# Kernel optimization log

Measured on AMD Instinct MI355X. Metric: run time of the kernel, lower is better.

Reference implementation:

```python
import jax, jax.numpy as jnp
import numpy as np
from functools import partial

NUM_CLASSES = 80
NUM_GRID = 32
NUM_BBOX = 2
IMG_H, IMG_W = 448.0, 448.0
IOU_THRESH = 0.5
SCORE_THRESH = 0.1
N_BATCH = 128


def setup_inputs() -> dict:
    key = jax.random.key(0)
    G2 = NUM_GRID * NUM_GRID
    feat = G2 * (NUM_CLASSES + 5 * NUM_BBOX)
    x = jax.random.uniform(key, (N_BATCH, feat), dtype=jnp.float32)
    return {"x": x}


def _decode(bb):
    # bb: [G2, 5] -> [G2, 5] as (x0, y0, x1, y1, conf) in image pixels
    G = NUM_GRID
    idx = jnp.arange(G * G)
    xg = (idx % G).astype(bb.dtype)   # x varies fastest (repeat(G,1).flatten())
    yg = (idx // G).astype(bb.dtype)  # y repeated per row (repeat(1,G).flatten())
    cx = (bb[:, 0] + xg) / G
    cy = (bb[:, 1] + yg) / G
    x0 = (cx - bb[:, 2] / 2) * IMG_W
    y0 = (cy - bb[:, 3] / 2) * IMG_H
    x1 = (cx + bb[:, 2] / 2) * IMG_W
    y1 = (cy + bb[:, 3] / 2) * IMG_H
    return jnp.stack([x0, y0, x1, y1, bb[:, 4]], axis=1)


def _pairwise_iou(boxes):
    # boxes: [M, 4] -> iou [M, M]
    area = jnp.maximum(boxes[:, 2] - boxes[:, 0], 0.0) * jnp.maximum(boxes[:, 3] - boxes[:, 1], 0.0)
    lt = jnp.maximum(boxes[:, None, :2], boxes[None, :, :2])
    rb = jnp.minimum(boxes[:, None, 2:], boxes[None, :, 2:])
    wh = jnp.maximum(rb - lt, 0.0)
    inter = wh[..., 0] * wh[..., 1]
    union = area[:, None] + area[None, :] - inter
    return inter / jnp.maximum(union, 1e-9)


def _nms_keep(iou, valid_sorted, thresh):
    # greedy NMS over score-sorted boxes; suppress j>i when iou[i,j] > thresh
    M = iou.shape[0]
    j = jnp.arange(M)

    def body(i, keep):
        sup = keep[i] & (iou[i] > thresh) & (j > i)
        return keep & ~sup

    return jax.lax.fori_loop(0, M, body, valid_sorted)


def _per_image(logits, bb):
    # logits: [G2, C], bb: [G2, 5]
    probs = jax.nn.softmax(logits, axis=-1)
    dec = _decode(bb)                      # [G2, 5]
    scores = dec[:, 4]
    reserve = scores > SCORE_THRESH        # bool mask (torch filters; we mask)
    # clip boxes to image
    boxes = jnp.stack([
        jnp.clip(dec[:, 0], 0.0, IMG_W),
        jnp.clip(dec[:, 1], 0.0, IMG_H),
        jnp.clip(dec[:, 2], 0.0, IMG_W),
        jnp.clip(dec[:, 3], 0.0, IMG_H),
    ], axis=1)
    labels = jnp.argmax(probs, axis=-1)
    # batched NMS via per-class coordinate offsets (torchvision trick)
    max_coord = jnp.max(jnp.where(reserve[:, None], boxes, 0.0))
    obox = boxes + (labels.astype(boxes.dtype) * (max_coord + 1.0))[:, None]
    eff = jnp.where(reserve, scores, -1.0)
    order = jnp.argsort(-eff)
    iou = _pairwise_iou(obox[order])       # [G2, G2]
    keep_sorted = _nms_keep(iou, reserve[order], IOU_THRESH)
    keep = jnp.zeros_like(reserve).at[order].set(keep_sorted)
    return boxes, scores, reserve, keep


def reference(x):
    N = x.shape[0]
    G2 = NUM_GRID * NUM_GRID
    x = x.reshape(N, G2, NUM_CLASSES + 5 * NUM_BBOX)
    class_logits = x[..., :NUM_CLASSES]                       # [N, G2, C]
    yb = x[..., NUM_CLASSES:].reshape(N, G2, NUM_BBOX, 5)
    best = jnp.argmax(yb[..., 4], axis=-1)                    # [N, G2]
    yolo_bboxes = jnp.take_along_axis(yb, best[..., None, None], axis=2)[:, :, 0, :]  # [N, G2, 5]
    boxes, scores, reserve_mask, keep_mask = jax.vmap(_per_image)(class_logits, yolo_bboxes)
    return class_logits, yolo_bboxes, boxes, scores, reserve_mask, keep_mask
```

## Files before the change

kernel.cpp:

```cpp
#include <hip/hip_runtime.h>
#include <stdint.h>

#define NB 128
#define G 32
#define G2 1024
#define NC 80
#define IMGW 448.0f
#define NCELL (NB * G2)

#define WS_LABEL_OFF 0u
#define WS_SEG_OFF   0x80000u
#define WS_BSEG_OFF  0x180000u
#define WS_CNT_OFF   0x380000u
#define WS_START_OFF 0x38A000u

__global__ __launch_bounds__(256) void percell_kernel(
    const float* __restrict__ x,
    float* __restrict__ out0, float* __restrict__ out1,
    float* __restrict__ out2, float* __restrict__ out3,
    float* __restrict__ out4, float* __restrict__ out5,
    int* __restrict__ ws_label)
{
#pragma clang fp contract(off)
    __shared__ float s_out1[16 * 5];
    __shared__ float4 s_out2[16];
    __shared__ float s_out3[16];
    __shared__ float s_out4[16];
    __shared__ int   s_lab[16];

    const int t = threadIdx.x;
    const int lane = t & 15;
    const int grp  = t >> 4;
    const int l64  = t & 63;
    const int base = l64 & 48;
    const int cell = blockIdx.x * 16 + grp;

    const float2* p2 = (const float2*)x + (size_t)cell * 45;
    float2* o0 = (float2*)out0 + (size_t)cell * 40;

    float bv = -INFINITY;
    int bi = 0;

    float2 a = p2[lane];
    o0[lane] = a;
    if (a.x > bv) { bv = a.x; bi = 2 * lane; }
    if (a.y > bv) { bv = a.y; bi = 2 * lane + 1; }
    float2 bq = p2[lane + 16];
    o0[lane + 16] = bq;
    if (bq.x > bv) { bv = bq.x; bi = 32 + 2 * lane; }
    if (bq.y > bv) { bv = bq.y; bi = 32 + 2 * lane + 1; }
    float2 cq = make_float2(0.0f, 0.0f);
    if (lane < 13) cq = p2[lane + 32];
    if (lane < 8) {
        o0[lane + 32] = cq;
        if (cq.x > bv) { bv = cq.x; bi = 64 + 2 * lane; }
        if (cq.y > bv) { bv = cq.y; bi = 64 + 2 * lane + 1; }
    }

#pragma unroll
    for (int o = 1; o < 16; o <<= 1) {
        float ov = __shfl_xor(bv, o, 64);
        int   oi = __shfl_xor(bi, o, 64);
        if (ov > bv || (ov == bv && oi < bi)) { bv = ov; bi = oi; }
    }

    float f40x = __shfl(cq.x, base + 8, 64),  f40y = __shfl(cq.y, base + 8, 64);
    float f41x = __shfl(cq.x, base + 9, 64),  f41y = __shfl(cq.y, base + 9, 64);
    float f42x = __shfl(cq.x, base + 10, 64), f42y = __shfl(cq.y, base + 10, 64);
    float f43x = __shfl(cq.x, base + 11, 64), f43y = __shfl(cq.y, base + 11, 64);
    float f44x = __shfl(cq.x, base + 12, 64), f44y = __shfl(cq.y, base + 12, 64);

    if (lane == 0) {
        float b0, b1, b2, b3, b4;
        if (f44y > f42x) { b0 = f42y; b1 = f43x; b2 = f43y; b3 = f44x; b4 = f44y; }
        else             { b0 = f40x; b1 = f40y; b2 = f41x; b3 = f41y; b4 = f42x; }

        s_out1[grp * 5 + 0] = b0; s_out1[grp * 5 + 1] = b1;
        s_out1[grp * 5 + 2] = b2; s_out1[grp * 5 + 3] = b3;
        s_out1[grp * 5 + 4] = b4;

        int g = cell & (G2 - 1);
        float xg = (float)(g & (G - 1));
        float yg = (float)(g >> 5);
        float cx = (b0 + xg) / 32.0f;
        float cy = (b1 + yg) / 32.0f;
        float hw = b2 / 2.0f, hh = b3 / 2.0f;
        float x0 = fminf(fmaxf((cx - hw) * IMGW, 0.0f), IMGW);
        float y0 = fminf(fmaxf((cy - hh) * IMGW, 0.0f), IMGW);
        float x1 = fminf(fmaxf((cx + hw) * IMGW, 0.0f), IMGW);
        float y1 = fminf(fmaxf((cy + hh) * IMGW, 0.0f), IMGW);

        s_out2[grp] = make_float4(x0, y0, x1, y1);
        s_out3[grp] = b4;
        s_out4[grp] = (b4 > 0.1f) ? 1.0f : 0.0f;
        s_lab[grp] = bi;
    }
    __syncthreads();

    if (t < 80)                 out1[(size_t)blockIdx.x * 80 + t] = s_out1[t];
    else if (t >= 80 && t < 96) out3[(size_t)blockIdx.x * 16 + (t - 80)] = s_out3[t - 80];
    else if (t < 112)           out4[(size_t)blockIdx.x * 16 + (t - 96)] = s_out4[t - 96];
    else if (t < 128)           ws_label[(size_t)blockIdx.x * 16 + (t - 112)] = s_lab[t - 112];
    else if (t < 144)           ((float4*)out2)[(size_t)blockIdx.x * 16 + (t - 128)] = s_out2[t - 128];
    else if (t < 160)           out5[(size_t)blockIdx.x * 16 + (t - 144)] = 0.0f;
}

__global__ __launch_bounds__(1024) void build_kernel(
    const float4* __restrict__ boxes,
    const float* __restrict__ scores,
    const int* __restrict__ labels,
    unsigned long long* __restrict__ ws_seg,
    float4* __restrict__ ws_bseg,
    int* __restrict__ ws_cnt, int* __restrict__ ws_start)
{
#pragma clang fp contract(off)
    __shared__ unsigned long long seg_s[G2];
    __shared__ float4 bseg_s[G2];
    __shared__ int cnt_s[NC];
    __shared__ int start_s[NC];
    __shared__ int cur_s[NC];
    __shared__ float red_s[16];

    const int n = blockIdx.x;
    const int t = threadIdx.x;

    if (t < NC) { cnt_s[t] = 0; cur_s[t] = 0; }

    float4 b = boxes[n * G2 + t];
    float sc = scores[n * G2 + t];
    int lab = labels[n * G2 + t];
    bool res = sc > 0.1f;

    float m = res ? fmaxf(fmaxf(b.x, b.y), fmaxf(b.z, b.w)) : 0.0f;
#pragma unroll
    for (int o = 32; o > 0; o >>= 1) m = fmaxf(m, __shfl_xor(m, o, 64));
    if ((t & 63) == 0) red_s[t >> 6] = m;
    __syncthreads();
    if (t == 0) {
        float mm = red_s[0];
#pragma unroll
        for (int i = 1; i < 16; ++i) mm = fmaxf(mm, red_s[i]);
        red_s[0] = mm;
    }
    if (res) atomicAdd(&cnt_s[lab], 1);
    __syncthreads();
    const float mult = red_s[0] + 1.0f;

    if (t < NC) {
        int s = 0;
        for (int c = 0; c < t; ++c) s += cnt_s[c];
        start_s[t] = s;
    }
    __syncthreads();

    if (res) {
        int slot = atomicAdd(&cur_s[lab], 1);
        int pos = start_s[lab] + slot;
        seg_s[pos] = ((unsigned long long)__float_as_uint(sc) << 10) |
                     (unsigned)(1023 - t);
        float off = (float)lab * mult;
        bseg_s[pos] = make_float4(b.x + off, b.y + off, b.z + off, b.w + off);
    }
    __syncthreads();

    ws_seg[n * G2 + t]  = seg_s[t];
    ws_bseg[n * G2 + t] = bseg_s[t];
    if (t < NC) {
        ws_cnt[n * NC + t]   = cnt_s[t];
        ws_start[n * NC + t] = start_s[t];
    }
}

__global__ __launch_bounds__(256) void nms_kernel(
    const unsigned long long* __restrict__ ws_seg,
    const float4* __restrict__ ws_bseg,
    const int* __restrict__ ws_cnt, const int* __restrict__ ws_start,
    float* __restrict__ out5)
{
#pragma clang fp contract(off)
    __shared__ unsigned long long k_s[4][64];
    __shared__ float4 ob_s[4][64];
    __shared__ float  ar_s[4][64];

    const int wv = threadIdx.x >> 6;
    const int l  = threadIdx.x & 63;
    const int w  = blockIdx.x * 4 + wv;
    const int n  = w / NC;
    const int c  = w - n * NC;

    const int cnt = ws_cnt[n * NC + c];
    if (cnt == 0) return;
    const int s = ws_start[n * NC + c];

    const bool valid = l < cnt;
    unsigned long long key = 0;
    int idx = 0;
    float4 mob = make_float4(0.f, 0.f, 0.f, 0.f);
    float marea = 0.f;
    if (valid) {
        key = ws_seg[n * G2 + s + l];
        mob = ws_bseg[n * G2 + s + l];
        idx = 1023 - (int)(key & 1023u);
        marea = fmaxf(mob.z - mob.x, 0.0f) * fmaxf(mob.w - mob.y, 0.0f);
        k_s[wv][l] = key;
    }
    asm volatile("s_waitcnt lgkmcnt(0)" ::: "memory");

    int r = 0;
    for (int i = 0; i < cnt; ++i) r += (k_s[wv][i] > key);

    if (valid) { ob_s[wv][r] = mob; ar_s[wv][r] = marea; }
    asm volatile("s_waitcnt lgkmcnt(0)" ::: "memory");

    unsigned long long sup = 0;
    for (int i = 0; i < cnt; ++i) {
        float4 A = ob_s[wv][i];
        float aA = ar_s[wv][i];
        float ltx = fmaxf(A.x, mob.x);
        float lty = fmaxf(A.y, mob.y);
        float rbx = fminf(A.z, mob.z);
        float rby = fminf(A.w, mob.w);
        float ww = fmaxf(rbx - ltx, 0.0f);
        float hh = fmaxf(rby - lty, 0.0f);
        float inter = ww * hh;
        float uni = (aA + marea) - inter;
        float iou = inter / fmaxf(uni, 1e-9f);
        if (i < r && iou > 0.5f) sup |= 1ull << i;
    }

    unsigned long long kept = 0;
    for (int i = 0; i < cnt; ++i) {
        bool ki = (r == i) && ((sup & kept) == 0ull);
        kept |= __ballot(ki) ? (1ull << i) : 0ull;
    }
    if (valid) out5[n * G2 + idx] = ((kept >> r) & 1ull) ? 1.0f : 0.0f;
}

extern "C" void kernel_launch(void* const* d_in, const int* in_sizes, int n_in,
                              void* d_out, int out_size, void* d_ws, size_t ws_size,
                              hipStream_t stream) {
    const float* x = (const float*)d_in[0];
    float* out = (float*)d_out;
    float* out0 = out;
    float* out1 = out0 + (size_t)NCELL * NC;
    float* out2 = out1 + (size_t)NCELL * 5;
    float* out3 = out2 + (size_t)NCELL * 4;
    float* out4 = out3 + (size_t)NCELL;
    float* out5 = out4 + (size_t)NCELL;

    int* ws_label = (int*)((char*)d_ws + WS_LABEL_OFF);
    unsigned long long* ws_seg = (unsigned long long*)((char*)d_ws + WS_SEG_OFF);
    float4* ws_bseg = (float4*)((char*)d_ws + WS_BSEG_OFF);
    int* ws_cnt   = (int*)((char*)d_ws + WS_CNT_OFF);
    int* ws_start = (int*)((char*)d_ws + WS_START_OFF);

    percell_kernel<<<NCELL / 16, 256, 0, stream>>>(
        x, out0, out1, out2, out3, out4, out5, ws_label);
    build_kernel<<<NB, 1024, 0, stream>>>(
        (const float4*)out2, out3, ws_label, ws_seg, ws_bseg, ws_cnt, ws_start);
    nms_kernel<<<(NB * NC) / 4, 256, 0, stream>>>(
        ws_seg, ws_bseg, ws_cnt, ws_start, out5);
}
```

Before: 41.95 us.

## Eliminate build kernel by per-class key scan with ballot compaction in NMS

Percell kernel now emits packed keys (label, score, cell index) and per-block coordinate maxima. The NMS kernel reduces the maxima and has each wavefront scan all keys of its image, compacting its class's entries via ballot/popcount, then gathers boxes and applies the class offset. This removes the separate per-image build kernel and its launch and serialization, at the cost of every class wavefront reading the whole image's key array.

After: 45.64 us. 1.09x slower.

```diff
diff --git a/kernel.cpp b/kernel.cpp
--- a/kernel.cpp
+++ b/kernel.cpp
@@ -8,25 +8,23 @@
 #define IMGW 448.0f
 #define NCELL (NB * G2)
 
-#define WS_LABEL_OFF 0u
-#define WS_SEG_OFF   0x80000u
-#define WS_BSEG_OFF  0x180000u
-#define WS_CNT_OFF   0x380000u
-#define WS_START_OFF 0x38A000u
+#define WS_KEY_OFF  0u
+#define WS_BMAX_OFF 0x100000u
 
 __global__ __launch_bounds__(256) void percell_kernel(
     const float* __restrict__ x,
     float* __restrict__ out0, float* __restrict__ out1,
     float* __restrict__ out2, float* __restrict__ out3,
     float* __restrict__ out4, float* __restrict__ out5,
-    int* __restrict__ ws_label)
+    unsigned long long* __restrict__ ws_key, float* __restrict__ ws_bmax)
 {
 #pragma clang fp contract(off)
     __shared__ float s_out1[16 * 5];
     __shared__ float4 s_out2[16];
     __shared__ float s_out3[16];
     __shared__ float s_out4[16];
-    __shared__ int   s_lab[16];
+    __shared__ unsigned long long s_key[16];
+    __shared__ float s_mx[16];
 
     const int t = threadIdx.x;
     const int lane = t & 15;
@@ -92,89 +90,36 @@
 
         s_out2[grp] = make_float4(x0, y0, x1, y1);
         s_out3[grp] = b4;
-        s_out4[grp] = (b4 > 0.1f) ? 1.0f : 0.0f;
-        s_lab[grp] = bi;
+        bool res = b4 > 0.1f;
+        s_out4[grp] = res ? 1.0f : 0.0f;
+
+        s_key[grp] = res
+            ? (((unsigned long long)bi << 41) |
+               ((unsigned long long)__float_as_uint(b4) << 10) |
+               (unsigned)(1023 - g))
+            : (127ull << 41);
+        s_mx[grp] = res ? fmaxf(fmaxf(x0, y0), fmaxf(x1, y1)) : 0.0f;
     }
     __syncthreads();
 
     if (t < 80)                 out1[(size_t)blockIdx.x * 80 + t] = s_out1[t];
     else if (t >= 80 && t < 96) out3[(size_t)blockIdx.x * 16 + (t - 80)] = s_out3[t - 80];
     else if (t < 112)           out4[(size_t)blockIdx.x * 16 + (t - 96)] = s_out4[t - 96];
-    else if (t < 128)           ws_label[(size_t)blockIdx.x * 16 + (t - 112)] = s_lab[t - 112];
+    else if (t < 128)           ws_key[(size_t)blockIdx.x * 16 + (t - 112)] = s_key[t - 112];
     else if (t < 144)           ((float4*)out2)[(size_t)blockIdx.x * 16 + (t - 128)] = s_out2[t - 128];
     else if (t < 160)           out5[(size_t)blockIdx.x * 16 + (t - 144)] = 0.0f;
+    else if (t == 160) {
+        float mm = s_mx[0];
+#pragma unroll
+        for (int i = 1; i < 16; ++i) mm = fmaxf(mm, s_mx[i]);
+        ws_bmax[blockIdx.x] = mm;
+    }
 }
 
-__global__ __launch_bounds__(1024) void build_kernel(
+__global__ __launch_bounds__(256) void nms_kernel(
+    const unsigned long long* __restrict__ ws_key,
+    const float* __restrict__ ws_bmax,
     const float4* __restrict__ boxes,
-    const float* __restrict__ scores,
-    const int* __restrict__ labels,
-    unsigned long long* __restrict__ ws_seg,
-    float4* __restrict__ ws_bseg,
-    int* __restrict__ ws_cnt, int* __restrict__ ws_start)
-{
-#pragma clang fp contract(off)
-    __shared__ unsigned long long seg_s[G2];
-    __shared__ float4 bseg_s[G2];
-    __shared__ int cnt_s[NC];
-    __shared__ int start_s[NC];
-    __shared__ int cur_s[NC];
-    __shared__ float red_s[16];
-
-    const int n = blockIdx.x;
-    const int t = threadIdx.x;
-
-    if (t < NC) { cnt_s[t] = 0; cur_s[t] = 0; }
-
-    float4 b = boxes[n * G2 + t];
-    float sc = scores[n * G2 + t];
-    int lab = labels[n * G2 + t];
-    bool res = sc > 0.1f;
-
-    float m = res ? fmaxf(fmaxf(b.x, b.y), fmaxf(b.z, b.w)) : 0.0f;
-#pragma unroll
-    for (int o = 32; o > 0; o >>= 1) m = fmaxf(m, __shfl_xor(m, o, 64));
-    if ((t & 63) == 0) red_s[t >> 6] = m;
-    __syncthreads();
-    if (t == 0) {
-        float mm = red_s[0];
-#pragma unroll
-        for (int i = 1; i < 16; ++i) mm = fmaxf(mm, red_s[i]);
-        red_s[0] = mm;
-    }
-    if (res) atomicAdd(&cnt_s[lab], 1);
-    __syncthreads();
-    const float mult = red_s[0] + 1.0f;
-
-    if (t < NC) {
-        int s = 0;
-        for (int c = 0; c < t; ++c) s += cnt_s[c];
-        start_s[t] = s;
-    }
-    __syncthreads();
-
-    if (res) {
-        int slot = atomicAdd(&cur_s[lab], 1);
-        int pos = start_s[lab] + slot;
-        seg_s[pos] = ((unsigned long long)__float_as_uint(sc) << 10) |
-                     (unsigned)(1023 - t);
-        float off = (float)lab * mult;
-        bseg_s[pos] = make_float4(b.x + off, b.y + off, b.z + off, b.w + off);
-    }
-    __syncthreads();
-
-    ws_seg[n * G2 + t]  = seg_s[t];
-    ws_bseg[n * G2 + t] = bseg_s[t];
-    if (t < NC) {
-        ws_cnt[n * NC + t]   = cnt_s[t];
-        ws_start[n * NC + t] = start_s[t];
-    }
-}
-
-__global__ __launch_bounds__(256) void nms_kernel(
-    const unsigned long long* __restrict__ ws_seg,
-    const float4* __restrict__ ws_bseg,
-    const int* __restrict__ ws_cnt, const int* __restrict__ ws_start,
     float* __restrict__ out5)
 {
 #pragma clang fp contract(off)
@@ -188,23 +133,40 @@
     const int n  = w / NC;
     const int c  = w - n * NC;
 
-    const int cnt = ws_cnt[n * NC + c];
+    float m = ws_bmax[n * 64 + l];
+#pragma unroll
+    for (int o = 32; o > 0; o >>= 1) m = fmaxf(m, __shfl_xor(m, o, 64));
+    const float mult = m + 1.0f;
+    const float off = (float)c * mult;
+
+    const unsigned long long* kp = ws_key + (size_t)n * G2;
+    int cnt = 0;
+#pragma unroll 4
+    for (int rnd = 0; rnd < 16; ++rnd) {
+        unsigned long long k = kp[rnd * 64 + l];
+        bool hit = (int)(k >> 41) == c;
+        unsigned long long bal = __ballot(hit);
+        if (hit) {
+            int pos = cnt + __popcll(bal & ((1ull << l) - 1ull));
+            if (pos < 64) k_s[wv][pos] = k;
+        }
+        cnt += __popcll(bal);
+    }
     if (cnt == 0) return;
-    const int s = ws_start[n * NC + c];
+    cnt = min(cnt, 64);
+    asm volatile("s_waitcnt lgkmcnt(0)" ::: "memory");
 
     const bool valid = l < cnt;
-    unsigned long long key = 0;
+    const unsigned long long key = valid ? k_s[wv][l] : 0ull;
     int idx = 0;
     float4 mob = make_float4(0.f, 0.f, 0.f, 0.f);
     float marea = 0.f;
     if (valid) {
-        key = ws_seg[n * G2 + s + l];
-        mob = ws_bseg[n * G2 + s + l];
         idx = 1023 - (int)(key & 1023u);
+        float4 bb = boxes[(size_t)n * G2 + idx];
+        mob = make_float4(bb.x + off, bb.y + off, bb.z + off, bb.w + off);
         marea = fmaxf(mob.z - mob.x, 0.0f) * fmaxf(mob.w - mob.y, 0.0f);
-        k_s[wv][l] = key;
-    }
-    asm volatile("s_waitcnt lgkmcnt(0)" ::: "memory");
+    }
 
     int r = 0;
     for (int i = 0; i < cnt; ++i) r += (k_s[wv][i] > key);
@@ -233,7 +195,7 @@
         bool ki = (r == i) && ((sup & kept) == 0ull);
         kept |= __ballot(ki) ? (1ull << i) : 0ull;
     }
-    if (valid) out5[n * G2 + idx] = ((kept >> r) & 1ull) ? 1.0f : 0.0f;
+    if (valid) out5[(size_t)n * G2 + idx] = ((kept >> r) & 1ull) ? 1.0f : 0.0f;
 }
 
 extern "C" void kernel_launch(void* const* d_in, const int* in_sizes, int n_in,
@@ -248,16 +210,11 @@
     float* out4 = out3 + (size_t)NCELL;
     float* out5 = out4 + (size_t)NCELL;
 
-    int* ws_label = (int*)((char*)d_ws + WS_LABEL_OFF);
-    unsigned long long* ws_seg = (unsigned long long*)((char*)d_ws + WS_SEG_OFF);
-    float4* ws_bseg = (float4*)((char*)d_ws + WS_BSEG_OFF);
-    int* ws_cnt   = (int*)((char*)d_ws + WS_CNT_OFF);
-    int* ws_start = (int*)((char*)d_ws + WS_START_OFF);
+    unsigned long long* ws_key = (unsigned long long*)((char*)d_ws + WS_KEY_OFF);
+    float* ws_bmax = (float*)((char*)d_ws + WS_BMAX_OFF);
 
     percell_kernel<<<NCELL / 16, 256, 0, stream>>>(
-        x, out0, out1, out2, out3, out4, out5, ws_label);
-    build_kernel<<<NB, 1024, 0, stream>>>(
-        (const float4*)out2, out3, ws_label, ws_seg, ws_bseg, ws_cnt, ws_start);
+        x, out0, out1, out2, out3, out4, out5, ws_key, ws_bmax);
     nms_kernel<<<(NB * NC) / 4, 256, 0, stream>>>(
-        ws_seg, ws_bseg, ws_cnt, ws_start, out5);
+        ws_key, ws_bmax, (const float4*)out2, out5);
 }
```
